# Kernel optimization log

Measured on AMD Instinct MI355X. Metric: run time of the kernel, lower is better.

## Reference

```python
import jax, jax.numpy as jnp
import numpy as np

DELTA_V = 0.5
DELTA_D = 1.5
LOSS_WEIGHT = 1.0


def setup_inputs() -> dict:
    key = jax.random.key(0)
    k1, k2, k3, k4 = jax.random.split(key, 4)
    B, D, H, W = 8, 4, 640, 640
    return {
        "emb": jax.random.normal(k1, (B, D, H, W), dtype=jnp.float32),
        "instance": jax.random.randint(k2, (B, H, W), 0, 33, dtype=jnp.int32),
        "kernel": jax.random.uniform(k3, (B, H, W), dtype=jnp.float32),
        "training_mask": jax.random.uniform(k4, (B, H, W), dtype=jnp.float32),
        "num_labels": 33,  # static: background label 0 + 32 instances, all present w.h.p.
    }


def _single(emb, instance, kernel, tmask, num_labels):
    # emb: [D,H,W]; instance: [H,W] int; kernel/tmask: [H,W] float
    D = emb.shape[0]
    tm = (tmask > 0.5).astype(instance.dtype)
    kn = (kernel > 0.5).astype(instance.dtype)
    inst2 = instance * tm                      # instance masked by training mask
    inst_k = (inst2 * kn).reshape(-1)          # kernel-restricted labels, [N]
    inst = inst2.reshape(-1)                   # [N]
    x = emb.reshape(D, -1).T                   # [N, D]
    ones = jnp.ones(x.shape[0], jnp.float32)

    # per-instance kernel means (scatter-mean), label 0 column forced to zero
    sums = jax.ops.segment_sum(x, inst_k, num_segments=num_labels)      # [K1, D]
    cnts = jax.ops.segment_sum(ones, inst_k, num_segments=num_labels)   # [K1]
    mean = sums / jnp.maximum(cnts, 1.0)[:, None]
    mean = mean.at[0].set(0.0)

    # aggregation term: per-pixel distance to its instance mean, segmented mean over labels 1..K
    diff = x - mean[inst]                                               # [N, D]
    dist = jnp.sqrt(jnp.sum(diff * diff, axis=1))
    val = jnp.log(jnp.maximum(dist - DELTA_V, 0.0) ** 2 + 1.0)
    cnt_i = jax.ops.segment_sum(ones, inst, num_segments=num_labels)
    agg = jax.ops.segment_sum(val, inst, num_segments=num_labels) / jnp.maximum(cnt_i, 1.0)
    l_agg = jnp.mean(agg[1:])

    # discrimination term: pairwise distances between instance means (exclude label 0 and diagonal)
    m = mean[1:]                                                        # [K, D]
    K = m.shape[0]
    pdiff = m[:, None, :] - m[None, :, :]
    pd = jnp.sqrt(jnp.sum(pdiff * pdiff, axis=-1) + jnp.eye(K))         # diag padded (masked below)
    vald = jnp.log(jnp.maximum(2.0 * DELTA_D - pd, 0.0) ** 2 + 1.0)
    off = 1.0 - jnp.eye(K)
    l_dis = jnp.sum(vald * off) / (K * (K - 1))

    # regularizer: mean over all num_labels columns; label-0 column contributes log(1)=0
    nrm1 = jnp.sqrt(jnp.sum(m * m, axis=1))
    l_reg = jnp.sum(jnp.log(nrm1 + 1.0)) / num_labels * 0.001

    return l_agg + l_dis + l_reg


def reference(emb, instance, kernel, training_mask, num_labels):
    f = lambda e, i, k, t: _single(e, i, k, t, num_labels)
    loss_batch = jax.vmap(f)(emb, instance, kernel, training_mask)
    return jnp.mean(LOSS_WEIGHT * loss_batch)
```

## Files before the change

### kernel.cpp

```cpp
#include <hip/hip_runtime.h>
#include <math.h>

#define HW    409600
#define HW4   102400
#define BATCH 8
#define NLAB  33
#define GXB   200
#define NREP  8
#define RS    201
#define MEANS_OFF 0
#define P2_OFF    2048
#define AWS_OFF   4096
#define P1_OFF    8192
#define LABS_OFF_F (P1_OFF + BATCH*GXB*200)
#define NEED_SPLIT ((size_t)LABS_OFF_F * 4)
#define NEED_LABS  ((size_t)LABS_OFF_F * 4 + (size_t)BATCH * HW4 * 4)

#if defined(__has_builtin) && __has_builtin(__builtin_amdgcn_sched_barrier)
#define SCHED_PIN() __builtin_amdgcn_sched_barrier(0)
#else
#define SCHED_PIN()
#endif

__global__ void init_aws(float* ws) {
    int i = blockIdx.x * 256 + threadIdx.x;
    if (i < BATCH * 208) ws[AWS_OFF + i] = 0.f;
}

__device__ __forceinline__ float getc(const float4& v, int e) {
    return (e == 0) ? v.x : (e == 1) ? v.y : (e == 2) ? v.z : v.w;
}
__device__ __forceinline__ float wave_sum(float v) {
    #pragma unroll
    for (int o = 32; o > 0; o >>= 1) v += __shfl_xor(v, o);
    return v;
}

struct Quad { int4 iv; float4 tv, kv, x0, x1, x2, x3; };

__device__ __forceinline__ void loadQ(Quad& q, const int4* inst4, const float4* tm4,
                                      const float4* kern4, const float4* emb4, int g) {
    q.iv = inst4[g];
    q.tv = tm4[g];
    q.kv = kern4[g];
    q.x0 = emb4[g];
    q.x1 = emb4[g + HW4];
    q.x2 = emb4[g + 2 * HW4];
    q.x3 = emb4[g + 3 * HW4];
}

__device__ __forceinline__ void acc1(int l, bool k,
                                     float x0, float x1, float x2, float x3,
                                     float* mb) {
    if (l) {
        float* bb = mb + l * 6;
        atomicAdd(bb + 5, 1.f);
        if (k) {
            atomicAdd(bb + 0, x0);
            atomicAdd(bb + 1, x1);
            atomicAdd(bb + 2, x2);
            atomicAdd(bb + 3, x3);
            atomicAdd(bb + 4, 1.f);
        }
    }
}

__device__ __forceinline__ void procQ(const Quad& q, float* mb,
                                      unsigned* labs, size_t labidx) {
    int l0 = (q.tv.x > 0.5f) ? q.iv.x : 0;
    int l1 = (q.tv.y > 0.5f) ? q.iv.y : 0;
    int l2 = (q.tv.z > 0.5f) ? q.iv.z : 0;
    int l3 = (q.tv.w > 0.5f) ? q.iv.w : 0;
    if (labs)
        labs[labidx] = (unsigned)l0 | ((unsigned)l1 << 8) |
                       ((unsigned)l2 << 16) | ((unsigned)l3 << 24);
    acc1(l0, q.kv.x > 0.5f, q.x0.x, q.x1.x, q.x2.x, q.x3.x, mb);
    acc1(l1, q.kv.y > 0.5f, q.x0.y, q.x1.y, q.x2.y, q.x3.y, mb);
    acc1(l2, q.kv.z > 0.5f, q.x0.z, q.x1.z, q.x2.z, q.x3.z, mb);
    acc1(l3, q.kv.w > 0.5f, q.x0.w, q.x1.w, q.x2.w, q.x3.w, mb);
}

template<bool SPLIT>
__global__ __launch_bounds__(256, 8) void pass1(const float* __restrict__ emb,
                                                const int*   __restrict__ inst,
                                                const float* __restrict__ kern,
                                                const float* __restrict__ tmask,
                                                float*       __restrict__ ws,
                                                unsigned*    __restrict__ labs) {
    __shared__ float bins[NREP][RS];
    const int t = threadIdx.x, bx = blockIdx.x, b = blockIdx.y;
    float* mb = bins[(t >> 3) & (NREP - 1)];

    const size_t  base  = (size_t)b * HW;
    const float4* emb4  = (const float4*)(emb + base * 4);
    const int4*   inst4 = (const int4*)(inst + base);
    const float4* kern4 = (const float4*)(kern + base);
    const float4* tm4   = (const float4*)(tmask + base);
    const int q0 = bx * 512 + t;
    const size_t lb = (size_t)b * HW4;

    for (int i = t; i < NREP * RS; i += 256) (&bins[0][0])[i] = 0.f;
    __syncthreads();

    Quad q;
    loadQ(q, inst4, tm4, kern4, emb4, q0);
    SCHED_PIN();
    procQ(q, mb, labs, lb + q0);
    loadQ(q, inst4, tm4, kern4, emb4, q0 + 256);
    SCHED_PIN();
    procQ(q, mb, labs, lb + q0 + 256);
    __syncthreads();

    if (t < NLAB * 6) {
        float v = 0.f;
        #pragma unroll
        for (int r = 0; r < NREP; ++r) v += bins[r][t];
        if (SPLIT) {
            ws[P1_OFF + ((size_t)b * GXB + bx) * 200 + t] = v;
        } else {
            if (v != 0.f) atomicAdd(ws + AWS_OFF + b * 208 + t, v);
        }
    }
}

template<bool SPLIT>
__global__ __launch_bounds__(256) void reduce_means(float* __restrict__ ws) {
    __shared__ float raw[200];
    const int t = threadIdx.x, b = blockIdx.x;
    if (t < NLAB * 6) {
        float s = 0.f;
        if (SPLIT) {
            const float* p = ws + P1_OFF + (size_t)b * GXB * 200 + t;
            float s0 = 0.f, s1 = 0.f, s2 = 0.f, s3 = 0.f;
            for (int bx = 0; bx < GXB; bx += 4) {
                s0 += p[(bx + 0) * 200];
                s1 += p[(bx + 1) * 200];
                s2 += p[(bx + 2) * 200];
                s3 += p[(bx + 3) * 200];
            }
            s = (s0 + s1) + (s2 + s3);
        } else {
            s = ws[AWS_OFF + b * 208 + t];
        }
        raw[t] = s;
    }
    __syncthreads();
    float* mm = ws + MEANS_OFF + b * 168;
    if (t < NLAB) {
        float cntk = raw[t * 6 + 4], cnti = raw[t * 6 + 5];
        float inv = 1.f / fmaxf(cntk, 1.f);
        float z = (t == 0) ? 0.f : 1.f;
        mm[t * 4 + 0] = z * raw[t * 6 + 0] * inv;
        mm[t * 4 + 1] = z * raw[t * 6 + 1] * inv;
        mm[t * 4 + 2] = z * raw[t * 6 + 2] * inv;
        mm[t * 4 + 3] = z * raw[t * 6 + 3] * inv;
        mm[132 + t]   = 1.f / fmaxf(cnti, 1.f);
    }
}

struct Quad2 { unsigned pk; int4 iv; float4 tv, x0, x1, x2, x3; };

template<bool USE_LABS>
__device__ __forceinline__ void loadQ2(Quad2& q, const unsigned* labs, size_t lb,
                                       const int4* inst4, const float4* tm4,
                                       const float4* emb4, int g) {
    if (USE_LABS) {
        q.pk = labs[lb + g];
    } else {
        q.iv = inst4[g];
        q.tv = tm4[g];
    }
    q.x0 = emb4[g];
    q.x1 = emb4[g + HW4];
    q.x2 = emb4[g + 2 * HW4];
    q.x3 = emb4[g + 3 * HW4];
}

template<bool USE_LABS>
__device__ __forceinline__ float procQ2(const Quad2& q, const float4* means4,
                                        const float* invci) {
    unsigned pk;
    if (USE_LABS) {
        pk = q.pk;
    } else {
        pk = (unsigned)((q.tv.x > 0.5f) ? q.iv.x : 0)        |
             ((unsigned)((q.tv.y > 0.5f) ? q.iv.y : 0) << 8) |
             ((unsigned)((q.tv.z > 0.5f) ? q.iv.z : 0) << 16)|
             ((unsigned)((q.tv.w > 0.5f) ? q.iv.w : 0) << 24);
    }
    float acc = 0.f;
    #pragma unroll
    for (int e = 0; e < 4; ++e) {
        int l = (pk >> (8 * e)) & 255;
        if (l) {
            float4 m = means4[l];
            float d0 = getc(q.x0, e) - m.x, d1 = getc(q.x1, e) - m.y;
            float d2 = getc(q.x2, e) - m.z, d3 = getc(q.x3, e) - m.w;
            float dist = sqrtf(d0 * d0 + d1 * d1 + d2 * d2 + d3 * d3);
            float u = fmaxf(dist - 0.5f, 0.f);
            acc += __logf(u * u + 1.f) * invci[l];
        }
    }
    return acc;
}

template<bool USE_LABS>
__global__ __launch_bounds__(256, 8) void pass2(const float* __restrict__ emb,
                                                const int*   __restrict__ inst,
                                                const float* __restrict__ tmask,
                                                float*       __restrict__ ws,
                                                const unsigned* __restrict__ labs) {
    __shared__ float4 means4[NLAB];
    __shared__ float  invci[NLAB];
    __shared__ float  red[4];
    const int t = threadIdx.x, bx = blockIdx.x, b = blockIdx.y;

    const size_t  base  = (size_t)b * HW;
    const float4* emb4  = (const float4*)(emb + base * 4);
    const int4*   inst4 = (const int4*)(inst + base);
    const float4* tm4   = (const float4*)(tmask + base);
    const int q0 = bx * 512 + t;
    const size_t lb = (size_t)b * HW4;

    Quad2 q;
    loadQ2<USE_LABS>(q, labs, lb, inst4, tm4, emb4, q0);
    SCHED_PIN();

    const float* mm = ws + MEANS_OFF + b * 168;
    if (t < NLAB) {
        means4[t] = ((const float4*)mm)[t];
        invci[t]  = mm[132 + t];
    }
    __syncthreads();

    float acc = procQ2<USE_LABS>(q, means4, invci);
    loadQ2<USE_LABS>(q, labs, lb, inst4, tm4, emb4, q0 + 256);
    SCHED_PIN();
    acc += procQ2<USE_LABS>(q, means4, invci);

    acc = wave_sum(acc);
    if ((t & 63) == 0) red[t >> 6] = acc;
    __syncthreads();
    if (t == 0)
        ws[P2_OFF + b * 256 + bx] = red[0] + red[1] + red[2] + red[3];
}

__global__ __launch_bounds__(256) void final_kernel(const float* __restrict__ ws,
                                                    float* __restrict__ out) {
    __shared__ float4 means4[NLAB];
    __shared__ float  red[4];
    const int t = threadIdx.x;
    float total = 0.f;
    for (int b = 0; b < BATCH; ++b) {
        __syncthreads();
        const float* mm = ws + MEANS_OFF + b * 168;
        if (t < NLAB) means4[t] = ((const float4*)mm)[t];
        __syncthreads();

        float part = (t < GXB) ? ws[P2_OFF + b * 256 + t] * (1.f / 32.f) : 0.f;
        float disp = 0.f;
        for (int p = t; p < 1024; p += 256) {
            int i = p >> 5, j = p & 31;
            if (i != j) {
                float4 mi = means4[i + 1], mj = means4[j + 1];
                float d0 = mi.x - mj.x, d1 = mi.y - mj.y;
                float d2 = mi.z - mj.z, d3 = mi.w - mj.w;
                float pd = sqrtf(d0 * d0 + d1 * d1 + d2 * d2 + d3 * d3);
                float u = fmaxf(3.0f - pd, 0.f);
                disp += __logf(u * u + 1.f);
            }
        }
        disp *= 1.f / 992.f;
        float regp = 0.f;
        if (t >= 1 && t < NLAB) {
            float4 m = means4[t];
            float n2 = m.x * m.x + m.y * m.y + m.z * m.z + m.w * m.w;
            regp = __logf(sqrtf(n2) + 1.f) * (0.001f / 33.f);
        }
        float v = wave_sum(part + disp + regp);
        if ((t & 63) == 0) red[t >> 6] = v;
        __syncthreads();
        if (t == 0) total += red[0] + red[1] + red[2] + red[3];
    }
    if (t == 0) out[0] = total * (1.f / BATCH);
}

extern "C" void kernel_launch(void* const* d_in, const int* in_sizes, int n_in,
                              void* d_out, int out_size, void* d_ws, size_t ws_size,
                              hipStream_t stream) {
    const float* emb   = (const float*)d_in[0];
    const int*   inst  = (const int*)  d_in[1];
    const float* kern  = (const float*)d_in[2];
    const float* tmask = (const float*)d_in[3];
    float* ws  = (float*)d_ws;
    float* out = (float*)d_out;

    const bool split    = ws_size >= NEED_SPLIT;
    const bool use_labs = ws_size >= NEED_LABS;
    unsigned* labs = use_labs ? (unsigned*)(ws + LABS_OFF_F) : nullptr;

    if (!split) init_aws<<<dim3((BATCH * 208 + 255) / 256), 256, 0, stream>>>(ws);
    dim3 grid(GXB, BATCH);
    if (split) pass1<true ><<<grid, 256, 0, stream>>>(emb, inst, kern, tmask, ws, labs);
    else       pass1<false><<<grid, 256, 0, stream>>>(emb, inst, kern, tmask, ws, labs);
    if (split) reduce_means<true ><<<BATCH, 256, 0, stream>>>(ws);
    else       reduce_means<false><<<BATCH, 256, 0, stream>>>(ws);
    if (use_labs) pass2<true ><<<grid, 256, 0, stream>>>(emb, inst, tmask, ws, labs);
    else          pass2<false><<<grid, 256, 0, stream>>>(emb, inst, tmask, ws, nullptr);
    final_kernel<<<1, 256, 0, stream>>>(ws, out);
}
```

Baseline: 162.4 us.

## Count labels via wave ballots instead of LDS atomics and transpose partials layout

Replaces the per-pixel LDS atomic increments for instance and kernel counts with wave-wide ballot and popcount per label, packed into per-thread registers and flushed with one atomic per lane. Only the four embedding sums still use LDS atomics, so bins shrink from 6 to 4 floats per label. The split partials are stored transposed (feature-major) so reduce_means can read them contiguously with a wave reduction. The 32-label ballot loop adds ALU work and register pressure, and occupancy is lowered to 6 waves per SIMD.

```diff
diff --git a/kernel.cpp b/kernel.cpp
--- a/kernel.cpp
+++ b/kernel.cpp
@@ -7,12 +7,12 @@
 #define NLAB  33
 #define GXB   200
 #define NREP  8
-#define RS    201
+#define RS4   137
 #define MEANS_OFF 0
 #define P2_OFF    2048
 #define AWS_OFF   4096
 #define P1_OFF    8192
-#define LABS_OFF_F (P1_OFF + BATCH*GXB*200)
+#define LABS_OFF_F (P1_OFF + BATCH*200*GXB)
 #define NEED_SPLIT ((size_t)LABS_OFF_F * 4)
 #define NEED_LABS  ((size_t)LABS_OFF_F * 4 + (size_t)BATCH * HW4 * 4)
 
@@ -49,46 +49,57 @@
     q.x3 = emb4[g + 3 * HW4];
 }
 
-__device__ __forceinline__ void acc1(int l, bool k,
-                                     float x0, float x1, float x2, float x3,
-                                     float* mb) {
-    if (l) {
-        float* bb = mb + l * 6;
-        atomicAdd(bb + 5, 1.f);
-        if (k) {
-            atomicAdd(bb + 0, x0);
-            atomicAdd(bb + 1, x1);
-            atomicAdd(bb + 2, x2);
-            atomicAdd(bb + 3, x3);
-            atomicAdd(bb + 4, 1.f);
-        }
-    }
-}
-
-__device__ __forceinline__ void procQ(const Quad& q, float* mb,
-                                      unsigned* labs, size_t labidx) {
+__device__ __forceinline__ void procQ(const Quad& q, float* mb, unsigned* cc,
+                                      unsigned* labs, size_t idx) {
     int l0 = (q.tv.x > 0.5f) ? q.iv.x : 0;
     int l1 = (q.tv.y > 0.5f) ? q.iv.y : 0;
     int l2 = (q.tv.z > 0.5f) ? q.iv.z : 0;
     int l3 = (q.tv.w > 0.5f) ? q.iv.w : 0;
     if (labs)
-        labs[labidx] = (unsigned)l0 | ((unsigned)l1 << 8) |
-                       ((unsigned)l2 << 16) | ((unsigned)l3 << 24);
-    acc1(l0, q.kv.x > 0.5f, q.x0.x, q.x1.x, q.x2.x, q.x3.x, mb);
-    acc1(l1, q.kv.y > 0.5f, q.x0.y, q.x1.y, q.x2.y, q.x3.y, mb);
-    acc1(l2, q.kv.z > 0.5f, q.x0.z, q.x1.z, q.x2.z, q.x3.z, mb);
-    acc1(l3, q.kv.w > 0.5f, q.x0.w, q.x1.w, q.x2.w, q.x3.w, mb);
+        labs[idx] = (unsigned)l0 | ((unsigned)l1 << 8) |
+                    ((unsigned)l2 << 16) | ((unsigned)l3 << 24);
+
+    bool k0 = q.kv.x > 0.5f, k1 = q.kv.y > 0.5f;
+    bool k2 = q.kv.z > 0.5f, k3 = q.kv.w > 0.5f;
+    unsigned long long km0 = __ballot(k0), km1 = __ballot(k1);
+    unsigned long long km2 = __ballot(k2), km3 = __ballot(k3);
+    #pragma unroll
+    for (int l = 1; l < NLAB; ++l) {
+        unsigned long long m0 = __ballot(l0 == l);
+        unsigned long long m1 = __ballot(l1 == l);
+        unsigned long long m2 = __ballot(l2 == l);
+        unsigned long long m3 = __ballot(l3 == l);
+        unsigned ci = (unsigned)(__popcll(m0) + __popcll(m1) +
+                                 __popcll(m2) + __popcll(m3));
+        unsigned ck = (unsigned)(__popcll(m0 & km0) + __popcll(m1 & km1) +
+                                 __popcll(m2 & km2) + __popcll(m3 & km3));
+        cc[l - 1] += ci + (ck << 16);
+    }
+    if (l0 && k0) { float* bb = mb + l0 * 4;
+        atomicAdd(bb, q.x0.x); atomicAdd(bb+1, q.x1.x);
+        atomicAdd(bb+2, q.x2.x); atomicAdd(bb+3, q.x3.x); }
+    if (l1 && k1) { float* bb = mb + l1 * 4;
+        atomicAdd(bb, q.x0.y); atomicAdd(bb+1, q.x1.y);
+        atomicAdd(bb+2, q.x2.y); atomicAdd(bb+3, q.x3.y); }
+    if (l2 && k2) { float* bb = mb + l2 * 4;
+        atomicAdd(bb, q.x0.z); atomicAdd(bb+1, q.x1.z);
+        atomicAdd(bb+2, q.x2.z); atomicAdd(bb+3, q.x3.z); }
+    if (l3 && k3) { float* bb = mb + l3 * 4;
+        atomicAdd(bb, q.x0.w); atomicAdd(bb+1, q.x1.w);
+        atomicAdd(bb+2, q.x2.w); atomicAdd(bb+3, q.x3.w); }
 }
 
 template<bool SPLIT>
-__global__ __launch_bounds__(256, 8) void pass1(const float* __restrict__ emb,
+__global__ __launch_bounds__(256, 6) void pass1(const float* __restrict__ emb,
                                                 const int*   __restrict__ inst,
                                                 const float* __restrict__ kern,
                                                 const float* __restrict__ tmask,
                                                 float*       __restrict__ ws,
                                                 unsigned*    __restrict__ labs) {
-    __shared__ float bins[NREP][RS];
+    __shared__ float    bins[NREP][RS4];
+    __shared__ unsigned cnts[NLAB];
     const int t = threadIdx.x, bx = blockIdx.x, b = blockIdx.y;
+    const unsigned lane = t & 63;
     float* mb = bins[(t >> 3) & (NREP - 1)];
 
     const size_t  base  = (size_t)b * HW;
@@ -99,27 +110,42 @@
     const int q0 = bx * 512 + t;
     const size_t lb = (size_t)b * HW4;
 
-    for (int i = t; i < NREP * RS; i += 256) (&bins[0][0])[i] = 0.f;
-    __syncthreads();
+    for (int i = t; i < NREP * RS4; i += 256) (&bins[0][0])[i] = 0.f;
+    if (t < NLAB) cnts[t] = 0u;
+    __syncthreads();
+
+    unsigned cc[NLAB - 1];
+    #pragma unroll
+    for (int l = 0; l < NLAB - 1; ++l) cc[l] = 0u;
 
     Quad q;
     loadQ(q, inst4, tm4, kern4, emb4, q0);
     SCHED_PIN();
-    procQ(q, mb, labs, lb + q0);
+    procQ(q, mb, cc, labs, lb + q0);
     loadQ(q, inst4, tm4, kern4, emb4, q0 + 256);
     SCHED_PIN();
-    procQ(q, mb, labs, lb + q0 + 256);
-    __syncthreads();
-
-    if (t < NLAB * 6) {
-        float v = 0.f;
+    procQ(q, mb, cc, labs, lb + q0 + 256);
+
+    unsigned vc = 0;
+    #pragma unroll
+    for (int l = 1; l < NLAB; ++l) vc = (lane == (unsigned)l) ? cc[l - 1] : vc;
+    if (lane >= 1 && lane < NLAB) atomicAdd(&cnts[lane], vc);
+    __syncthreads();
+
+    float v = 0.f;
+    if (t < 132) {
         #pragma unroll
         for (int r = 0; r < NREP; ++r) v += bins[r][t];
-        if (SPLIT) {
-            ws[P1_OFF + ((size_t)b * GXB + bx) * 200 + t] = v;
-        } else {
-            if (v != 0.f) atomicAdd(ws + AWS_OFF + b * 208 + t, v);
-        }
+    } else if (t < 165) {
+        v = (float)(cnts[t - 132] & 0xFFFFu);
+    } else if (t < 198) {
+        v = (float)(cnts[t - 165] >> 16);
+    }
+    if (t < 198) {
+        if (SPLIT)
+            ws[P1_OFF + ((size_t)b * 200 + t) * GXB + bx] = v;
+        else if (v != 0.f)
+            atomicAdd(ws + AWS_OFF + b * 208 + t, v);
     }
 }
 
@@ -127,34 +153,33 @@
 __global__ __launch_bounds__(256) void reduce_means(float* __restrict__ ws) {
     __shared__ float raw[200];
     const int t = threadIdx.x, b = blockIdx.x;
-    if (t < NLAB * 6) {
-        float s = 0.f;
-        if (SPLIT) {
-            const float* p = ws + P1_OFF + (size_t)b * GXB * 200 + t;
-            float s0 = 0.f, s1 = 0.f, s2 = 0.f, s3 = 0.f;
-            for (int bx = 0; bx < GXB; bx += 4) {
-                s0 += p[(bx + 0) * 200];
-                s1 += p[(bx + 1) * 200];
-                s2 += p[(bx + 2) * 200];
-                s3 += p[(bx + 3) * 200];
+    const int w = t >> 6, lane = t & 63;
+    if (SPLIT) {
+        for (int f = w; f < 198; f += 4) {
+            const float* p = ws + P1_OFF + ((size_t)b * 200 + f) * GXB;
+            float s = 0.f;
+            #pragma unroll
+            for (int base = 0; base < GXB; base += 64) {
+                int i = base + lane;
+                if (i < GXB) s += p[i];
             }
-            s = (s0 + s1) + (s2 + s3);
-        } else {
-            s = ws[AWS_OFF + b * 208 + t];
+            s = wave_sum(s);
+            if (lane == 0) raw[f] = s;
         }
-        raw[t] = s;
+    } else {
+        if (t < 198) raw[t] = ws[AWS_OFF + b * 208 + t];
     }
     __syncthreads();
     float* mm = ws + MEANS_OFF + b * 168;
     if (t < NLAB) {
-        float cntk = raw[t * 6 + 4], cnti = raw[t * 6 + 5];
-        float inv = 1.f / fmaxf(cntk, 1.f);
+        float ci = raw[132 + t], ck = raw[165 + t];
+        float inv = 1.f / fmaxf(ck, 1.f);
         float z = (t == 0) ? 0.f : 1.f;
-        mm[t * 4 + 0] = z * raw[t * 6 + 0] * inv;
-        mm[t * 4 + 1] = z * raw[t * 6 + 1] * inv;
-        mm[t * 4 + 2] = z * raw[t * 6 + 2] * inv;
-        mm[t * 4 + 3] = z * raw[t * 6 + 3] * inv;
-        mm[132 + t]   = 1.f / fmaxf(cnti, 1.f);
+        mm[t * 4 + 0] = z * raw[t * 4 + 0] * inv;
+        mm[t * 4 + 1] = z * raw[t * 4 + 1] * inv;
+        mm[t * 4 + 2] = z * raw[t * 4 + 2] * inv;
+        mm[t * 4 + 3] = z * raw[t * 4 + 3] * inv;
+        mm[132 + t]   = 1.f / fmaxf(ci, 1.f);
     }
 }
 
```

After: 183.6 us. +13.0%, slower.

## Stage pass inputs through LDS with async global_load_lds and halve block chunk

Applied to the files above, without the earlier changes.

Both passes now copy their input tiles (labels, masks, embedding channels) straight from global memory into shared memory using the AMD global-load-to-LDS builtin, then read them back from LDS. Each block now covers 1024 pixels instead of 2048, which doubles the grid to 400 blocks per image and changes the partial-sum layouts. The aim is to raise memory-level parallelism and cut register pressure on what is a bandwidth-bound loss kernel. In exchange it adds LDS traffic, more partial results to reduce, and lower occupancy bounds.

```diff
diff --git a/kernel.cpp b/kernel.cpp
--- a/kernel.cpp
+++ b/kernel.cpp
@@ -5,22 +5,17 @@
 #define HW4   102400
 #define BATCH 8
 #define NLAB  33
-#define GXB   200
+#define CH    1024
+#define NCH   (HW/CH)
 #define NREP  8
 #define RS    201
 #define MEANS_OFF 0
 #define P2_OFF    2048
-#define AWS_OFF   4096
+#define AWS_OFF   6144
 #define P1_OFF    8192
-#define LABS_OFF_F (P1_OFF + BATCH*GXB*200)
+#define LABS_OFF_F (P1_OFF + BATCH*NCH*200)
 #define NEED_SPLIT ((size_t)LABS_OFF_F * 4)
-#define NEED_LABS  ((size_t)LABS_OFF_F * 4 + (size_t)BATCH * HW4 * 4)
-
-#if defined(__has_builtin) && __has_builtin(__builtin_amdgcn_sched_barrier)
-#define SCHED_PIN() __builtin_amdgcn_sched_barrier(0)
-#else
-#define SCHED_PIN()
-#endif
+#define NEED_LABS  (NEED_SPLIT + (size_t)BATCH * HW4 * 4)
 
 __global__ void init_aws(float* ws) {
     int i = blockIdx.x * 256 + threadIdx.x;
@@ -36,17 +31,14 @@
     return v;
 }
 
-struct Quad { int4 iv; float4 tv, kv, x0, x1, x2, x3; };
-
-__device__ __forceinline__ void loadQ(Quad& q, const int4* inst4, const float4* tm4,
-                                      const float4* kern4, const float4* emb4, int g) {
-    q.iv = inst4[g];
-    q.tv = tm4[g];
-    q.kv = kern4[g];
-    q.x0 = emb4[g];
-    q.x1 = emb4[g + HW4];
-    q.x2 = emb4[g + 2 * HW4];
-    q.x3 = emb4[g + 3 * HW4];
+__device__ __forceinline__ void stage16(const unsigned* g, float* l, int lane) {
+#if defined(__has_builtin) && __has_builtin(__builtin_amdgcn_global_load_lds)
+    __builtin_amdgcn_global_load_lds(
+        (const __attribute__((address_space(1))) unsigned int*)(g + 4 * lane),
+        (__attribute__((address_space(3))) unsigned int*)l, 16, 0, 0);
+#else
+    ((uint4*)l)[lane] = ((const uint4*)g)[lane];
+#endif
 }
 
 __device__ __forceinline__ void acc1(int l, bool k,
@@ -65,61 +57,74 @@
     }
 }
 
-__device__ __forceinline__ void procQ(const Quad& q, float* mb,
-                                      unsigned* labs, size_t labidx) {
-    int l0 = (q.tv.x > 0.5f) ? q.iv.x : 0;
-    int l1 = (q.tv.y > 0.5f) ? q.iv.y : 0;
-    int l2 = (q.tv.z > 0.5f) ? q.iv.z : 0;
-    int l3 = (q.tv.w > 0.5f) ? q.iv.w : 0;
-    if (labs)
-        labs[labidx] = (unsigned)l0 | ((unsigned)l1 << 8) |
-                       ((unsigned)l2 << 16) | ((unsigned)l3 << 24);
-    acc1(l0, q.kv.x > 0.5f, q.x0.x, q.x1.x, q.x2.x, q.x3.x, mb);
-    acc1(l1, q.kv.y > 0.5f, q.x0.y, q.x1.y, q.x2.y, q.x3.y, mb);
-    acc1(l2, q.kv.z > 0.5f, q.x0.z, q.x1.z, q.x2.z, q.x3.z, mb);
-    acc1(l3, q.kv.w > 0.5f, q.x0.w, q.x1.w, q.x2.w, q.x3.w, mb);
-}
-
 template<bool SPLIT>
-__global__ __launch_bounds__(256, 8) void pass1(const float* __restrict__ emb,
+__global__ __launch_bounds__(256, 4) void pass1(const float* __restrict__ emb,
                                                 const int*   __restrict__ inst,
                                                 const float* __restrict__ kern,
                                                 const float* __restrict__ tmask,
                                                 float*       __restrict__ ws,
                                                 unsigned*    __restrict__ labs) {
+    __shared__ float stage[7 * CH];
     __shared__ float bins[NREP][RS];
     const int t = threadIdx.x, bx = blockIdx.x, b = blockIdx.y;
+    const int wave = t >> 6, lane = t & 63;
+
+    const size_t pixb = (size_t)bx * CH;
+    const unsigned* gs[7];
+    gs[0] = (const unsigned*)(inst  + (size_t)b * HW + pixb);
+    gs[1] = (const unsigned*)(tmask + (size_t)b * HW + pixb);
+    gs[2] = (const unsigned*)(kern  + (size_t)b * HW + pixb);
+    #pragma unroll
+    for (int d = 0; d < 4; ++d)
+        gs[3 + d] = (const unsigned*)(emb + ((size_t)b * 4 + d) * HW + pixb);
+
+    #pragma unroll
+    for (int i = 0; i < 7; ++i) {
+        int tau = wave * 7 + i;
+        int s = tau >> 2, p = tau & 3;
+        stage16(gs[s] + p * 256, &stage[s * CH + p * 256], lane);
+    }
+
     float* mb = bins[(t >> 3) & (NREP - 1)];
-
-    const size_t  base  = (size_t)b * HW;
-    const float4* emb4  = (const float4*)(emb + base * 4);
-    const int4*   inst4 = (const int4*)(inst + base);
-    const float4* kern4 = (const float4*)(kern + base);
-    const float4* tm4   = (const float4*)(tmask + base);
-    const int q0 = bx * 512 + t;
-    const size_t lb = (size_t)b * HW4;
-
     for (int i = t; i < NREP * RS; i += 256) (&bins[0][0])[i] = 0.f;
     __syncthreads();
 
-    Quad q;
-    loadQ(q, inst4, tm4, kern4, emb4, q0);
-    SCHED_PIN();
-    procQ(q, mb, labs, lb + q0);
-    loadQ(q, inst4, tm4, kern4, emb4, q0 + 256);
-    SCHED_PIN();
-    procQ(q, mb, labs, lb + q0 + 256);
-    __syncthreads();
-
-    if (t < NLAB * 6) {
+    const int4*   sI = (const int4*)  (stage + 0 * CH);
+    const float4* sT = (const float4*)(stage + 1 * CH);
+    const float4* sK = (const float4*)(stage + 2 * CH);
+    const float4* s0 = (const float4*)(stage + 3 * CH);
+    const float4* s1 = (const float4*)(stage + 4 * CH);
+    const float4* s2 = (const float4*)(stage + 5 * CH);
+    const float4* s3 = (const float4*)(stage + 6 * CH);
+
+    int4   iv = sI[t];
+    float4 tv = sT[t];
+    float4 kv = sK[t];
+    float4 x0 = s0[t], x1 = s1[t], x2 = s2[t], x3 = s3[t];
+
+    int l0 = (tv.x > 0.5f) ? iv.x : 0;
+    int l1 = (tv.y > 0.5f) ? iv.y : 0;
+    int l2 = (tv.z > 0.5f) ? iv.z : 0;
+    int l3 = (tv.w > 0.5f) ? iv.w : 0;
+    if (labs)
+        labs[(size_t)b * HW4 + (size_t)bx * (CH / 4) + t] =
+            (unsigned)l0 | ((unsigned)l1 << 8) |
+            ((unsigned)l2 << 16) | ((unsigned)l3 << 24);
+
+    acc1(l0, kv.x > 0.5f, x0.x, x1.x, x2.x, x3.x, mb);
+    acc1(l1, kv.y > 0.5f, x0.y, x1.y, x2.y, x3.y, mb);
+    acc1(l2, kv.z > 0.5f, x0.z, x1.z, x2.z, x3.z, mb);
+    acc1(l3, kv.w > 0.5f, x0.w, x1.w, x2.w, x3.w, mb);
+    __syncthreads();
+
+    if (t < 198) {
         float v = 0.f;
         #pragma unroll
         for (int r = 0; r < NREP; ++r) v += bins[r][t];
-        if (SPLIT) {
-            ws[P1_OFF + ((size_t)b * GXB + bx) * 200 + t] = v;
-        } else {
-            if (v != 0.f) atomicAdd(ws + AWS_OFF + b * 208 + t, v);
-        }
+        if (SPLIT)
+            ws[P1_OFF + ((size_t)b * NCH + bx) * 200 + t] = v;
+        else if (v != 0.f)
+            atomicAdd(ws + AWS_OFF + b * 208 + t, v);
     }
 }
 
@@ -127,18 +132,18 @@
 __global__ __launch_bounds__(256) void reduce_means(float* __restrict__ ws) {
     __shared__ float raw[200];
     const int t = threadIdx.x, b = blockIdx.x;
-    if (t < NLAB * 6) {
+    if (t < 198) {
         float s = 0.f;
         if (SPLIT) {
-            const float* p = ws + P1_OFF + (size_t)b * GXB * 200 + t;
-            float s0 = 0.f, s1 = 0.f, s2 = 0.f, s3 = 0.f;
-            for (int bx = 0; bx < GXB; bx += 4) {
-                s0 += p[(bx + 0) * 200];
-                s1 += p[(bx + 1) * 200];
-                s2 += p[(bx + 2) * 200];
-                s3 += p[(bx + 3) * 200];
+            const float* p = ws + P1_OFF + (size_t)b * NCH * 200 + t;
+            float a0 = 0, a1 = 0, a2 = 0, a3 = 0, a4 = 0, a5 = 0, a6 = 0, a7 = 0;
+            for (int i = 0; i < NCH; i += 8) {
+                a0 += p[(i + 0) * 200]; a1 += p[(i + 1) * 200];
+                a2 += p[(i + 2) * 200]; a3 += p[(i + 3) * 200];
+                a4 += p[(i + 4) * 200]; a5 += p[(i + 5) * 200];
+                a6 += p[(i + 6) * 200]; a7 += p[(i + 7) * 200];
             }
-            s = (s0 + s1) + (s2 + s3);
+            s = ((a0 + a1) + (a2 + a3)) + ((a4 + a5) + (a6 + a7));
         } else {
             s = ws[AWS_OFF + b * 208 + t];
         }
@@ -147,102 +152,95 @@
     __syncthreads();
     float* mm = ws + MEANS_OFF + b * 168;
     if (t < NLAB) {
-        float cntk = raw[t * 6 + 4], cnti = raw[t * 6 + 5];
-        float inv = 1.f / fmaxf(cntk, 1.f);
+        float ck = raw[t * 6 + 4], ci = raw[t * 6 + 5];
+        float inv = 1.f / fmaxf(ck, 1.f);
         float z = (t == 0) ? 0.f : 1.f;
         mm[t * 4 + 0] = z * raw[t * 6 + 0] * inv;
         mm[t * 4 + 1] = z * raw[t * 6 + 1] * inv;
         mm[t * 4 + 2] = z * raw[t * 6 + 2] * inv;
         mm[t * 4 + 3] = z * raw[t * 6 + 3] * inv;
-        mm[132 + t]   = 1.f / fmaxf(cnti, 1.f);
-    }
-}
-
-struct Quad2 { unsigned pk; int4 iv; float4 tv, x0, x1, x2, x3; };
+        mm[132 + t]   = 1.f / fmaxf(ci, 1.f);
+    }
+}
 
 template<bool USE_LABS>
-__device__ __forceinline__ void loadQ2(Quad2& q, const unsigned* labs, size_t lb,
-                                       const int4* inst4, const float4* tm4,
-                                       const float4* emb4, int g) {
+__global__ __launch_bounds__(256, 6) void pass2(const float* __restrict__ emb,
+                                                const int*   __restrict__ inst,
+                                                const float* __restrict__ tmask,
+                                                float*       __restrict__ ws,
+                                                const unsigned* __restrict__ labs) {
+    __shared__ float  stage[4 * CH + CH / 4];
+    __shared__ float4 means4[NLAB];
+    __shared__ float  invci[NLAB];
+    __shared__ float  red[4];
+    const int t = threadIdx.x, bx = blockIdx.x, b = blockIdx.y;
+    const int wave = t >> 6, lane = t & 63;
+    const size_t pixb = (size_t)bx * CH;
+
+    unsigned pk = 0;
+    float4 x0, x1, x2, x3;
     if (USE_LABS) {
-        q.pk = labs[lb + g];
+        const unsigned* gp[5];
+        #pragma unroll
+        for (int d = 0; d < 4; ++d)
+            gp[d] = (const unsigned*)(emb + ((size_t)b * 4 + d) * HW + pixb);
+        gp[4] = labs + (size_t)b * HW4 + (size_t)bx * (CH / 4);
+        for (int tau = wave; tau < 17; tau += 4) {
+            if (tau < 16) {
+                int s = tau >> 2, p = tau & 3;
+                stage16(gp[s] + p * 256, &stage[s * CH + p * 256], lane);
+            } else {
+                stage16(gp[4], &stage[4 * CH], lane);
+            }
+        }
     } else {
-        q.iv = inst4[g];
-        q.tv = tm4[g];
-    }
-    q.x0 = emb4[g];
-    q.x1 = emb4[g + HW4];
-    q.x2 = emb4[g + 2 * HW4];
-    q.x3 = emb4[g + 3 * HW4];
-}
-
-template<bool USE_LABS>
-__device__ __forceinline__ float procQ2(const Quad2& q, const float4* means4,
-                                        const float* invci) {
-    unsigned pk;
+        const float4* emb4  = (const float4*)(emb + (size_t)b * 4 * HW);
+        const int4*   inst4 = (const int4*)(inst + (size_t)b * HW);
+        const float4* tm4   = (const float4*)(tmask + (size_t)b * HW);
+        const int gq = bx * (CH / 4) + t;
+        int4 iv = inst4[gq]; float4 tv = tm4[gq];
+        pk = (unsigned)((tv.x > 0.5f) ? iv.x : 0)        |
+             ((unsigned)((tv.y > 0.5f) ? iv.y : 0) << 8) |
+             ((unsigned)((tv.z > 0.5f) ? iv.z : 0) << 16)|
+             ((unsigned)((tv.w > 0.5f) ? iv.w : 0) << 24);
+        x0 = emb4[gq]; x1 = emb4[gq + HW4];
+        x2 = emb4[gq + 2 * HW4]; x3 = emb4[gq + 3 * HW4];
+    }
+
+    const float* mm = ws + MEANS_OFF + b * 168;
+    if (t < NLAB) {
+        means4[t] = ((const float4*)mm)[t];
+        invci[t]  = mm[132 + t];
+    }
+    __syncthreads();
+
     if (USE_LABS) {
-        pk = q.pk;
-    } else {
-        pk = (unsigned)((q.tv.x > 0.5f) ? q.iv.x : 0)        |
-             ((unsigned)((q.tv.y > 0.5f) ? q.iv.y : 0) << 8) |
-             ((unsigned)((q.tv.z > 0.5f) ? q.iv.z : 0) << 16)|
-             ((unsigned)((q.tv.w > 0.5f) ? q.iv.w : 0) << 24);
-    }
+        pk = ((const unsigned*)(stage + 4 * CH))[t];
+        x0 = ((const float4*)(stage + 0 * CH))[t];
+        x1 = ((const float4*)(stage + 1 * CH))[t];
+        x2 = ((const float4*)(stage + 2 * CH))[t];
+        x3 = ((const float4*)(stage + 3 * CH))[t];
+    }
+
     float acc = 0.f;
     #pragma unroll
     for (int e = 0; e < 4; ++e) {
         int l = (pk >> (8 * e)) & 255;
         if (l) {
             float4 m = means4[l];
-            float d0 = getc(q.x0, e) - m.x, d1 = getc(q.x1, e) - m.y;
-            float d2 = getc(q.x2, e) - m.z, d3 = getc(q.x3, e) - m.w;
+            float d0 = getc(x0, e) - m.x, d1 = getc(x1, e) - m.y;
+            float d2 = getc(x2, e) - m.z, d3 = getc(x3, e) - m.w;
             float dist = sqrtf(d0 * d0 + d1 * d1 + d2 * d2 + d3 * d3);
             float u = fmaxf(dist - 0.5f, 0.f);
             acc += __logf(u * u + 1.f) * invci[l];
         }
     }
-    return acc;
-}
-
-template<bool USE_LABS>
-__global__ __launch_bounds__(256, 8) void pass2(const float* __restrict__ emb,
-                                                const int*   __restrict__ inst,
-                                                const float* __restrict__ tmask,
-                                                float*       __restrict__ ws,
-                                                const unsigned* __restrict__ labs) {
-    __shared__ float4 means4[NLAB];
-    __shared__ float  invci[NLAB];
-    __shared__ float  red[4];
-    const int t = threadIdx.x, bx = blockIdx.x, b = blockIdx.y;
-
-    const size_t  base  = (size_t)b * HW;
-    const float4* emb4  = (const float4*)(emb + base * 4);
-    const int4*   inst4 = (const int4*)(inst + base);
-    const float4* tm4   = (const float4*)(tmask + base);
-    const int q0 = bx * 512 + t;
-    const size_t lb = (size_t)b * HW4;
-
-    Quad2 q;
-    loadQ2<USE_LABS>(q, labs, lb, inst4, tm4, emb4, q0);
-    SCHED_PIN();
-
-    const float* mm = ws + MEANS_OFF + b * 168;
-    if (t < NLAB) {
-        means4[t] = ((const float4*)mm)[t];
-        invci[t]  = mm[132 + t];
-    }
-    __syncthreads();
-
-    float acc = procQ2<USE_LABS>(q, means4, invci);
-    loadQ2<USE_LABS>(q, labs, lb, inst4, tm4, emb4, q0 + 256);
-    SCHED_PIN();
-    acc += procQ2<USE_LABS>(q, means4, invci);
 
     acc = wave_sum(acc);
     if ((t & 63) == 0) red[t >> 6] = acc;
     __syncthreads();
     if (t == 0)
-        ws[P2_OFF + b * 256 + bx] = red[0] + red[1] + red[2] + red[3];
+        ws[P2_OFF + b * 512 + bx] = red[0] + red[1] + red[2] + red[3];
 }
 
 __global__ __launch_bounds__(256) void final_kernel(const float* __restrict__ ws,
@@ -257,7 +255,9 @@
         if (t < NLAB) means4[t] = ((const float4*)mm)[t];
         __syncthreads();
 
-        float part = (t < GXB) ? ws[P2_OFF + b * 256 + t] * (1.f / 32.f) : 0.f;
+        float pa = 0.f;
+        for (int i = t; i < NCH; i += 256) pa += ws[P2_OFF + b * 512 + i];
+        pa *= (1.f / 32.f);
         float disp = 0.f;
         for (int p = t; p < 1024; p += 256) {
             int i = p >> 5, j = p & 31;
@@ -277,7 +277,7 @@
             float n2 = m.x * m.x + m.y * m.y + m.z * m.z + m.w * m.w;
             regp = __logf(sqrtf(n2) + 1.f) * (0.001f / 33.f);
         }
-        float v = wave_sum(part + disp + regp);
+        float v = wave_sum(pa + disp + regp);
         if ((t & 63) == 0) red[t >> 6] = v;
         __syncthreads();
         if (t == 0) total += red[0] + red[1] + red[2] + red[3];
@@ -300,7 +300,7 @@
     unsigned* labs = use_labs ? (unsigned*)(ws + LABS_OFF_F) : nullptr;
 
     if (!split) init_aws<<<dim3((BATCH * 208 + 255) / 256), 256, 0, stream>>>(ws);
-    dim3 grid(GXB, BATCH);
+    dim3 grid(NCH, BATCH);
     if (split) pass1<true ><<<grid, 256, 0, stream>>>(emb, inst, kern, tmask, ws, labs);
     else       pass1<false><<<grid, 256, 0, stream>>>(emb, inst, kern, tmask, ws, labs);
     if (split) reduce_means<true ><<<BATCH, 256, 0, stream>>>(ws);
```

Result: slower. 167.0 us (+2.8%).
